# Kernel tuning notes

Measured on AMD Instinct MI355X. Metric: run time of the kernel, lower is better.

The kernel has to match this reference:

```python
import jax, jax.numpy as jnp
import numpy as np

B, L, D, H = 4, 2048, 512, 8
DH = D // H

def cdist(x):
    # torch.cdist(x, x) with p=2: (b,l,l) euclidean distances over feature dim
    sq = jnp.sum(x * x, axis=-1)  # (b,l)
    d2 = sq[:, :, None] + sq[:, None, :] - 2.0 * jnp.einsum('bld,bmd->blm', x, x)
    return jnp.sqrt(jnp.maximum(d2, 0.0))

def distance_residual_bias(cd, mask2d):
    # raw_max=True branch
    Dm = cd * mask2d
    row_max = jnp.max(Dm, axis=-1, keepdims=True)  # (b,l,1)
    Dm = row_max - Dm
    eye = jnp.eye(Dm.shape[-1], dtype=Dm.dtype)
    Dm = Dm * (1.0 - eye)  # zero diagonal
    return Dm * mask2d

def layernorm(x, g, b, eps=1e-5):
    mu = jnp.mean(x, axis=-1, keepdims=True)
    var = jnp.mean((x - mu) ** 2, axis=-1, keepdims=True)
    return (x - mu) * jax.lax.rsqrt(var + eps) * g + b

def setup_inputs() -> dict:
    key = jax.random.key(0)
    ks = jax.random.split(key, 16)
    s = lambda k, shape: jax.random.normal(k, shape, dtype=jnp.float32) * 0.02
    inp = {
        'x': jax.random.normal(ks[0], (B, L, D), dtype=jnp.float32),
        'node_mask': jnp.ones((B, L), dtype=jnp.float32),
        'wq': s(ks[1], (D, D)), 'bq': jnp.zeros((D,), jnp.float32),
        'wk': s(ks[2], (D, D)), 'bk': jnp.zeros((D,), jnp.float32),
        'wv': s(ks[3], (D, D)), 'bv': jnp.zeros((D,), jnp.float32),
        'wo': s(ks[4], (D, D)), 'bo': jnp.zeros((D,), jnp.float32),
        'ln1_g': jnp.ones((D,), jnp.float32), 'ln1_b': jnp.zeros((D,), jnp.float32),
        'w1': s(ks[5], (D, 4 * D)), 'b1': jnp.zeros((4 * D,), jnp.float32),
        'w2': s(ks[6], (4 * D, D)), 'b2': jnp.zeros((D,), jnp.float32),
        'ln2_g': jnp.ones((D,), jnp.float32), 'ln2_b': jnp.zeros((D,), jnp.float32),
    }
    return inp

def reference(x, node_mask, wq, bq, wk, bk, wv, bv, wo, bo,
              ln1_g, ln1_b, w1, b1, w2, b2, ln2_g, ln2_b):
    b, l, d = x.shape
    mask2d = node_mask[:, :, None] * node_mask[:, None, :]  # (b,l,l)
    bias = distance_residual_bias(cdist(x), mask2d)          # (b,l,l)

    q = (x @ wq + bq).reshape(b, l, H, DH).transpose(0, 2, 1, 3)
    k = (x @ wk + bk).reshape(b, l, H, DH).transpose(0, 2, 1, 3)
    v = (x @ wv + bv).reshape(b, l, H, DH).transpose(0, 2, 1, 3)
    scores = jnp.einsum('bhqd,bhkd->bhqk', q, k) / jnp.sqrt(jnp.float32(DH))
    scores = scores + bias[:, None, :, :]  # broadcast distance bias over heads
    attn = jax.nn.softmax(scores, axis=-1)
    y = jnp.einsum('bhqk,bhkd->bhqd', attn, v).transpose(0, 2, 1, 3).reshape(b, l, d)
    y = y @ wo + bo

    X = layernorm(x + y, ln1_g, ln1_b)            # AddNorm 1 (dropout=eval/no-op)
    ffn = jax.nn.relu(X @ w1 + b1) @ w2 + b2      # PositionWiseFFN
    X = layernorm(X + ffn, ln2_g, ln2_b)          # AddNorm 2
    return X
```

## Files before the change

kernel.cpp:

```cpp
#include <hip/hip_runtime.h>
#include <stdint.h>

#define GAS __attribute__((address_space(1)))
#define LAS __attribute__((address_space(3)))

typedef __attribute__((ext_vector_type(8))) __bf16 bf16x8;
typedef __attribute__((ext_vector_type(4))) float f32x4;

static constexpr int Bb = 4, Ll = 2048, Dd = 512, Hh = 8, DHd = 64;
static constexpr float LOG2E = 1.4426950408889634f;

__device__ __forceinline__ unsigned short f2bf(float f){
  unsigned u = __float_as_uint(f);
  u += 0x7fffu + ((u >> 16) & 1u);
  return (unsigned short)(u >> 16);
}
__device__ __forceinline__ float bf2f(unsigned short s){
  return __uint_as_float(((unsigned)s) << 16);
}
__device__ __forceinline__ void gload16(const void* g, void* l){
  __builtin_amdgcn_global_load_lds((const GAS void*)g, (LAS void*)l, 16, 0, 0);
}
__device__ __forceinline__ f32x4 mfma16(bf16x8 a, bf16x8 b, f32x4 c){
  return __builtin_amdgcn_mfma_f32_16x16x32_bf16(a, b, c, 0, 0, 0);
}
__device__ __forceinline__ float exp2_hw(float x){
  float r; asm("v_exp_f32 %0, %1" : "=v"(r) : "v"(x)); return r;
}

__global__ __launch_bounds__(256) void sumsq_cast(const float* __restrict__ x,
                                                  unsigned short* __restrict__ xbf,
                                                  float* __restrict__ sq){
  int row = blockIdx.x, tid = threadIdx.x;
  float2 v = ((const float2*)(x + (size_t)row * Dd))[tid];
  ((unsigned*)(xbf + (size_t)row * Dd))[tid] =
      (unsigned)f2bf(v.x) | ((unsigned)f2bf(v.y) << 16);
  float s2 = v.x * v.x + v.y * v.y;
  #pragma unroll
  for (int t = 1; t < 64; t <<= 1) s2 += __shfl_xor(s2, t, 64);
  __shared__ float red[4];
  if ((tid & 63) == 0) red[tid >> 6] = s2;
  __syncthreads();
  if (tid == 0) sq[row] = red[0] + red[1] + red[2] + red[3];
}

__global__ void transpose_all(
    const float* __restrict__ wq, const float* __restrict__ wk,
    const float* __restrict__ wv, const float* __restrict__ wo,
    const float* __restrict__ w1, const float* __restrict__ w2,
    unsigned short* __restrict__ wqkvT, unsigned short* __restrict__ woT,
    unsigned short* __restrict__ w1T, unsigned short* __restrict__ w2T)
{
  __shared__ float t[32][33];
  int bid = blockIdx.x;
  const float* in; unsigned short* out; int R, C, bx, by;
  if (bid < 1024){
    int s = bid >> 8, tt = bid & 255;
    in  = s == 0 ? wq : s == 1 ? wk : s == 2 ? wv : wo;
    out = s == 3 ? woT : wqkvT + s * 512 * 512;
    R = 512; C = 512; bx = tt & 15; by = tt >> 4;
  } else if (bid < 2048){
    int tt = bid - 1024; in = w1; out = w1T; R = 512; C = 2048; bx = tt & 63; by = tt >> 6;
  } else {
    int tt = bid - 2048; in = w2; out = w2T; R = 2048; C = 512; bx = tt & 15; by = tt >> 4;
  }
  int tx = threadIdx.x, ty = threadIdx.y;
  int c0 = bx * 32, r0 = by * 32;
  #pragma unroll
  for (int j = 0; j < 32; j += 8) t[ty + j][tx] = in[(size_t)(r0 + ty + j) * C + c0 + tx];
  __syncthreads();
  #pragma unroll
  for (int j = 0; j < 32; j += 8) out[(size_t)(c0 + ty + j) * R + r0 + tx] = f2bf(t[tx][ty + j]);
}

__global__ __launch_bounds__(256) void v_transpose(const unsigned short* __restrict__ qkv,
                                                   unsigned short* __restrict__ vT){
  int b = blockIdx.z, h = blockIdx.y, l0 = blockIdx.x * 64;
  int tid = threadIdx.x;
  __shared__ unsigned short t[64 * 64];
  #pragma unroll
  for (int it = 0; it < 2; ++it){
    int row = tid >> 2;
    int c = (tid & 3) + it * 4;
    uint4 d = *(const uint4*)(qkv + (size_t)(b * Ll + l0 + row) * 1536 + 1024 + h * DHd + c * 8);
    *(uint4*)((char*)t + row * 128 + ((c ^ (row & 7)) << 4)) = d;
  }
  __syncthreads();
  #pragma unroll
  for (int it = 0; it < 2; ++it){
    int dh = tid >> 2;
    int c2 = (tid & 3) + it * 4;
    unsigned pk[4];
    #pragma unroll
    for (int p = 0; p < 4; ++p){
      unsigned short e0, e1;
      {
        int ll = c2 * 8 + p * 2;
        e0 = *(const unsigned short*)((const char*)t + ll * 128 +
              ((((dh >> 3) ^ (ll & 7))) << 4) + ((dh & 7) << 1));
        ll = c2 * 8 + p * 2 + 1;
        e1 = *(const unsigned short*)((const char*)t + ll * 128 +
              ((((dh >> 3) ^ (ll & 7))) << 4) + ((dh & 7) << 1));
      }
      pk[p] = (unsigned)e0 | ((unsigned)e1 << 16);
    }
    uint4 o; o.x = pk[0]; o.y = pk[1]; o.z = pk[2]; o.w = pk[3];
    *(uint4*)(vT + ((size_t)(b * Hh + h) * DHd + dh) * Ll + l0 + c2 * 8) = o;
  }
}

template<int MODE>
__global__ __launch_bounds__(256) void gemm_bt(
    const unsigned short* __restrict__ A,
    const unsigned short* __restrict__ Bt,
    int M, int N, int K,
    const float* __restrict__ bias,
    const float* __restrict__ extra,
    float* __restrict__ outf,
    unsigned short* __restrict__ outb,
    const float* __restrict__ sq,
    float* __restrict__ rmax,
    const float* __restrict__ mask,
    const float* __restrict__ bias_k,
    const float* __restrict__ bias_v)
{
  if (MODE == 0){
    int z = blockIdx.z;
    A    += (size_t)z * Ll * Dd;
    Bt    = A;
    outb += (size_t)z * Ll * Ll;
    sq += z * Ll; rmax += z * Ll; mask += z * Ll;
  }
  const int m0 = blockIdx.y * 128, n0 = blockIdx.x * 128;
  const int tid = threadIdx.x, w = tid >> 6, l = tid & 63;
  const int wm = w >> 1, wn = w & 1;
  __shared__ unsigned short lA[2][128 * 64];
  __shared__ unsigned short lB[2][128 * 64];
  f32x4 acc[4][4];
  const f32x4 z4 = {0.f, 0.f, 0.f, 0.f};
  #pragma unroll
  for (int i = 0; i < 4; i++){
    #pragma unroll
    for (int j = 0; j < 4; j++) acc[i][j] = z4;
  }
  const int srow = w * 8 + (l >> 3);
  const int sc = l & 7;

  #pragma unroll
  for (int j = 0; j < 4; j++){
    int row = j * 32 + srow;
    gload16(A + (size_t)(m0 + row) * K + ((sc ^ (row & 7)) << 3),
            &lA[0][0] + j * 2048 + w * 512);
    gload16(Bt + (size_t)(n0 + row) * K + ((sc ^ (row & 7)) << 3),
            &lB[0][0] + j * 2048 + w * 512);
  }
  __syncthreads();

  int cur = 0;
  for (int k0 = 0; k0 < K; k0 += 64, cur ^= 1){
    if (k0 + 64 < K){
      #pragma unroll
      for (int j = 0; j < 4; j++){
        int row = j * 32 + srow;
        gload16(A + (size_t)(m0 + row) * K + k0 + 64 + ((sc ^ (row & 7)) << 3),
                &lA[cur ^ 1][0] + j * 2048 + w * 512);
        gload16(Bt + (size_t)(n0 + row) * K + k0 + 64 + ((sc ^ (row & 7)) << 3),
                &lB[cur ^ 1][0] + j * 2048 + w * 512);
      }
    }
    bf16x8 af[4][2], bv[4][2];
    #pragma unroll
    for (int kk = 0; kk < 2; kk++){
      #pragma unroll
      for (int f = 0; f < 4; f++){
        int ra = wm * 64 + f * 16 + (l & 15);
        af[f][kk] = *(const bf16x8*)((const char*)&lA[cur][0] + ra * 128 +
                      (((kk * 4 + (l >> 4)) ^ (ra & 7)) << 4));
        int rb = wn * 64 + f * 16 + (l & 15);
        bv[f][kk] = *(const bf16x8*)((const char*)&lB[cur][0] + rb * 128 +
                      (((kk * 4 + (l >> 4)) ^ (rb & 7)) << 4));
      }
    }
    #pragma unroll
    for (int mf = 0; mf < 4; mf++){
      #pragma unroll
      for (int nf = 0; nf < 4; nf++){
        #pragma unroll
        for (int kk = 0; kk < 2; kk++)
          acc[mf][nf] = mfma16(af[mf][kk], bv[nf][kk], acc[mf][nf]);
      }
    }
    __syncthreads();
  }

  #pragma unroll
  for (int mf = 0; mf < 4; mf++){
    #pragma unroll
    for (int r = 0; r < 4; r++){
      int row = m0 + wm * 64 + mf * 16 + (l >> 4) * 4 + r;
      if (MODE == 0){
        float sqi = sq[row];
        float mi  = mask[row];
        float rm = 0.f;
        #pragma unroll
        for (int nf = 0; nf < 4; nf++){
          int col = n0 + wn * 64 + nf * 16 + (l & 15);
          float g  = acc[mf][nf][r];
          float d2 = sqi + sq[col] - 2.f * g;
          float cd = sqrtf(fmaxf(d2, 0.f));
          float cdm = cd * (mi * mask[col]) * LOG2E;
          outb[(size_t)row * Ll + col] = f2bf(cdm);
          rm = fmaxf(rm, cdm);
        }
        #pragma unroll
        for (int t = 1; t < 16; t <<= 1) rm = fmaxf(rm, __shfl_xor(rm, t, 64));
        if ((l & 15) == 0) atomicMax((int*)(rmax + row), __float_as_int(rm));
      } else {
        #pragma unroll
        for (int nf = 0; nf < 4; nf++){
          int col = n0 + wn * 64 + nf * 16 + (l & 15);
          float bval;
          if (MODE == 5){
            const float* bp = col < 512 ? bias : (col < 1024 ? bias_k : bias_v);
            bval = bp[col & 511];
          } else {
            bval = bias[col];
          }
          float v = acc[mf][nf][r] + bval;
          if (MODE == 3) outb[(size_t)row * N + col] = f2bf(fmaxf(v, 0.f));
          if (MODE == 5) outb[(size_t)row * N + col] = f2bf(v);
          if (MODE == 2 || MODE == 4)
            outf[(size_t)row * N + col] = v + extra[(size_t)row * N + col];
        }
      }
    }
  }
}

__global__ __launch_bounds__(256) void flash_attn(
    const unsigned short* __restrict__ qkv,
    const unsigned short* __restrict__ vT,
    const unsigned short* __restrict__ cdm,
    const float* __restrict__ rmax,
    unsigned short* __restrict__ y)
{
  const int b = blockIdx.z, h = blockIdx.y, q0 = blockIdx.x * 64;
  const int tid = threadIdx.x, w = tid >> 6, l = tid & 63;
  const int ql = l & 15, lg = l >> 4;
  __shared__ unsigned short QPs[64 * 64];
  __shared__ unsigned short Ks[2][64 * 64];
  __shared__ unsigned short Vs[2][64 * 64];

  const int srow = w * 8 + (l >> 3);
  const int sc = l & 7;
  const unsigned short* kbase = qkv + (size_t)b * Ll * 1536 + 512 + h * DHd;
  const unsigned short* vbase = vT + (size_t)(b * Hh + h) * DHd * Ll;

  #pragma unroll
  for (int j = 0; j < 2; j++){
    int row = j * 32 + srow;
    gload16(qkv + (size_t)(b * Ll + q0 + row) * 1536 + h * DHd + ((sc ^ (row & 7)) << 3),
            QPs + j * 2048 + w * 512);
    gload16(kbase + (size_t)row * 1536 + ((sc ^ (row & 7)) << 3),
            &Ks[0][0] + j * 2048 + w * 512);
    gload16(vbase + (size_t)row * Ll + ((sc ^ (row & 7)) << 3),
            &Vs[0][0] + j * 2048 + w * 512);
  }

  const int qg = q0 + w * 16 + ql;
  const float rmx = rmax[b * Ll + qg];
  const unsigned short* cdrow = cdm + (size_t)(b * Ll + qg) * Ll;

  uint2 cdn[4];
  #pragma unroll
  for (int nf = 0; nf < 4; nf++)
    cdn[nf] = *(const uint2*)(cdrow + nf * 16 + lg * 4);

  f32x4 o[4];
  const f32x4 z4 = {0.f, 0.f, 0.f, 0.f};
  #pragma unroll
  for (int nf = 0; nf < 4; nf++) o[nf] = z4;
  float mprev = -1e30f, lsum = 0.f;

  __syncthreads();

  bf16x8 qa[2];
  #pragma unroll
  for (int kk = 0; kk < 2; kk++){
    int ra = w * 16 + ql;
    qa[kk] = *(const bf16x8*)((const char*)QPs + ra * 128 +
               (((kk * 4 + lg) ^ (ql & 7)) << 4));
  }

  const int NT = Ll / 64;
  for (int t = 0; t < NT; ++t){
    const int k0 = t * 64;
    const int cur = t & 1;

    uint2 cdc[4];
    #pragma unroll
    for (int nf = 0; nf < 4; nf++) cdc[nf] = cdn[nf];

    if (t + 1 < NT){
      const int kn = k0 + 64;
      #pragma unroll
      for (int nf = 0; nf < 4; nf++)
        cdn[nf] = *(const uint2*)(cdrow + kn + nf * 16 + lg * 4);
      #pragma unroll
      for (int j = 0; j < 2; j++){
        int row = j * 32 + srow;
        gload16(kbase + (size_t)(kn + row) * 1536 + ((sc ^ (row & 7)) << 3),
                &Ks[cur ^ 1][0] + j * 2048 + w * 512);
        gload16(vbase + (size_t)row * Ll + kn + ((sc ^ (row & 7)) << 3),
                &Vs[cur ^ 1][0] + j * 2048 + w * 512);
      }
    }

    f32x4 s[4];
    #pragma unroll
    for (int nf = 0; nf < 4; nf++){
      s[nf] = z4;
      #pragma unroll
      for (int kk = 0; kk < 2; kk++){
        int rb = nf * 16 + ql;
        bf16x8 kb = *(const bf16x8*)((const char*)Ks[cur] + rb * 128 +
                      (((kk * 4 + lg) ^ (ql & 7)) << 4));
        s[nf] = mfma16(kb, qa[kk], s[nf]);
      }
    }

    float sv[16];
    #pragma unroll
    for (int nf = 0; nf < 4; nf++){
      float c0 = __uint_as_float(cdc[nf].x << 16);
      float c1 = __uint_as_float(cdc[nf].x & 0xffff0000u);
      float c2 = __uint_as_float(cdc[nf].y << 16);
      float c3 = __uint_as_float(cdc[nf].y & 0xffff0000u);
      sv[nf * 4 + 0] = fmaf(s[nf][0], 0.125f * LOG2E, -c0);
      sv[nf * 4 + 1] = fmaf(s[nf][1], 0.125f * LOG2E, -c1);
      sv[nf * 4 + 2] = fmaf(s[nf][2], 0.125f * LOG2E, -c2);
      sv[nf * 4 + 3] = fmaf(s[nf][3], 0.125f * LOG2E, -c3);
    }
    if (k0 == q0){
      #pragma unroll
      for (int nf = 0; nf < 4; nf++) if (nf == w){
        #pragma unroll
        for (int r = 0; r < 4; r++)
          if (lg * 4 + r == ql) sv[nf * 4 + r] -= rmx;
      }
    }

    float tm = sv[0];
    #pragma unroll
    for (int i = 1; i < 16; i++) tm = fmaxf(tm, sv[i]);
    tm = fmaxf(tm, __shfl_xor(tm, 16, 64));
    tm = fmaxf(tm, __shfl_xor(tm, 32, 64));

    if (__any(tm > mprev + 8.f)){
      float mnew = fmaxf(mprev, tm);
      float a_ = exp2_hw(mprev - mnew);
      mprev = mnew;
      lsum *= a_;
      float al[4];
      #pragma unroll
      for (int r = 0; r < 4; r++)
        al[r] = __shfl(a_, (l & 48) | (lg * 4 + r), 64);
      #pragma unroll
      for (int nf = 0; nf < 4; nf++){
        f32x4 tv = o[nf];
        tv[0] *= al[0]; tv[1] *= al[1]; tv[2] *= al[2]; tv[3] *= al[3];
        o[nf] = tv;
      }
    }

    float p[16], ps = 0.f;
    #pragma unroll
    for (int i = 0; i < 16; i++){ p[i] = exp2_hw(sv[i] - mprev); ps += p[i]; }
    lsum += ps;

    #pragma unroll
    for (int nf = 0; nf < 4; nf++){
      unsigned d0, d1;
      asm("v_cvt_pk_bf16_f32 %0, %1, %2" : "=v"(d0) : "v"(p[nf*4+0]), "v"(p[nf*4+1]));
      asm("v_cvt_pk_bf16_f32 %0, %1, %2" : "=v"(d1) : "v"(p[nf*4+2]), "v"(p[nf*4+3]));
      uint2 pk2; pk2.x = d0; pk2.y = d1;
      *(uint2*)((char*)QPs + w * 2048 + ql * 128 +
                ((nf * 32 + lg * 8) ^ ((ql & 7) << 4))) = pk2;
    }

    bf16x8 pa[2];
    #pragma unroll
    for (int kk = 0; kk < 2; kk++)
      pa[kk] = *(const bf16x8*)((const char*)QPs + w * 2048 + ql * 128 +
                 ((((kk * 4 + lg)) ^ (ql & 7)) << 4));
    #pragma unroll
    for (int nf = 0; nf < 4; nf++){
      #pragma unroll
      for (int kk = 0; kk < 2; kk++){
        int rv = nf * 16 + ql;
        bf16x8 vb = *(const bf16x8*)((const char*)Vs[cur] + rv * 128 +
                      (((kk * 4 + lg) ^ (ql & 7)) << 4));
        o[nf] = mfma16(pa[kk], vb, o[nf]);
      }
    }
    __syncthreads();
  }

  float ltot = lsum;
  ltot += __shfl_xor(ltot, 16, 64);
  ltot += __shfl_xor(ltot, 32, 64);
  float lf[4];
  #pragma unroll
  for (int r = 0; r < 4; r++)
    lf[r] = __shfl(ltot, (l & 48) | (lg * 4 + r), 64);
  #pragma unroll
  for (int nf = 0; nf < 4; nf++){
    #pragma unroll
    for (int r = 0; r < 4; r++){
      int qo = q0 + w * 16 + lg * 4 + r;
      float v = o[nf][r] / lf[r];
      y[(size_t)(b * Ll + qo) * Dd + h * DHd + nf * 16 + ql] = f2bf(v);
    }
  }
}

__global__ __launch_bounds__(256) void ln_kernel(const float* __restrict__ in,
                                                 const float* __restrict__ g,
                                                 const float* __restrict__ bt,
                                                 float* __restrict__ outf,
                                                 unsigned short* __restrict__ outb){
  int row = blockIdx.x, tid = threadIdx.x;
  float2 v = ((const float2*)(in + (size_t)row * Dd))[tid];
  float s = v.x + v.y, s2 = v.x * v.x + v.y * v.y;
  #pragma unroll
  for (int t = 1; t < 64; t <<= 1){ s += __shfl_xor(s, t, 64); s2 += __shfl_xor(s2, t, 64); }
  __shared__ float red[8];
  if ((tid & 63) == 0){ red[tid >> 6] = s; red[4 + (tid >> 6)] = s2; }
  __syncthreads();
  float S  = red[0] + red[1] + red[2] + red[3];
  float S2 = red[4] + red[5] + red[6] + red[7];
  float mu = S * (1.f / 512.f);
  float var = fmaxf(S2 * (1.f / 512.f) - mu * mu, 0.f);
  float rs = rsqrtf(var + 1e-5f);
  int c = tid * 2;
  float o0 = (v.x - mu) * rs * g[c] + bt[c];
  float o1 = (v.y - mu) * rs * g[c + 1] + bt[c + 1];
  float2 ov; ov.x = o0; ov.y = o1;
  ((float2*)(outf + (size_t)row * Dd))[tid] = ov;
  if (outb){
    ((unsigned*)(outb + (size_t)row * Dd))[tid] =
        (unsigned)f2bf(o0) | ((unsigned)f2bf(o1) << 16);
  }
}

extern "C" void kernel_launch(void* const* d_in, const int* in_sizes, int n_in,
                              void* d_out, int out_size, void* d_ws, size_t ws_size,
                              hipStream_t stream){
  const float* x     = (const float*)d_in[0];
  const float* nmask = (const float*)d_in[1];
  const float* wq = (const float*)d_in[2];  const float* bq = (const float*)d_in[3];
  const float* wk = (const float*)d_in[4];  const float* bk = (const float*)d_in[5];
  const float* wv = (const float*)d_in[6];  const float* bv = (const float*)d_in[7];
  const float* wo = (const float*)d_in[8];  const float* bo = (const float*)d_in[9];
  const float* ln1g = (const float*)d_in[10]; const float* ln1b = (const float*)d_in[11];
  const float* w1 = (const float*)d_in[12]; const float* b1 = (const float*)d_in[13];
  const float* w2 = (const float*)d_in[14]; const float* b2 = (const float*)d_in[15];
  const float* ln2g = (const float*)d_in[16]; const float* ln2b = (const float*)d_in[17];
  float* outp = (float*)d_out;
  char* ws = (char*)d_ws;

  unsigned short* xbf   = (unsigned short*)(ws + 0);
  float* sq   = (float*)(ws + 8388608);
  float* rmax = (float*)(ws + 8421376);
  unsigned short* wqkvT = (unsigned short*)(ws + 8454144);
  unsigned short* woT   = (unsigned short*)(ws + 10027008);
  unsigned short* w1T   = (unsigned short*)(ws + 10551296);
  unsigned short* w2T   = (unsigned short*)(ws + 12648448);
  unsigned short* cdm   = (unsigned short*)(ws + 14745600);
  unsigned short* qkv   = (unsigned short*)(ws + 48300032);
  unsigned short* vT    = (unsigned short*)(ws + 73465856);
  unsigned short* yb    = (unsigned short*)(ws + 81854464);
  float* res = (float*)(ws + 90243072);
  float* Xf  = (float*)(ws + 107020288);
  unsigned short* h1  = cdm;
  unsigned short* Xbf = qkv;

  hipMemsetAsync(rmax, 0, sizeof(float) * Bb * Ll, stream);

  sumsq_cast<<<Bb * Ll, 256, 0, stream>>>(x, xbf, sq);

  transpose_all<<<3072, dim3(32, 8), 0, stream>>>(wq, wk, wv, wo, w1, w2,
                                                  wqkvT, woT, w1T, w2T);

  gemm_bt<0><<<dim3(16, 16, 4), 256, 0, stream>>>(xbf, xbf, Ll, Ll, Dd,
      nullptr, nullptr, nullptr, cdm, sq, rmax, nmask, nullptr, nullptr);

  gemm_bt<5><<<dim3(12, 64, 1), 256, 0, stream>>>(xbf, wqkvT, Bb * Ll, 1536, Dd,
      bq, nullptr, nullptr, qkv, nullptr, nullptr, nullptr, bk, bv);

  v_transpose<<<dim3(Ll / 64, Hh, Bb), 256, 0, stream>>>(qkv, vT);

  flash_attn<<<dim3(Ll / 64, Hh, Bb), 256, 0, stream>>>(qkv, vT, cdm, rmax, yb);

  gemm_bt<2><<<dim3(4, 64, 1), 256, 0, stream>>>(yb, woT, Bb * Ll, Dd, Dd,
      bo, x, res, nullptr, nullptr, nullptr, nullptr, nullptr, nullptr);

  ln_kernel<<<Bb * Ll, 256, 0, stream>>>(res, ln1g, ln1b, Xf, Xbf);

  gemm_bt<3><<<dim3(16, 64, 1), 256, 0, stream>>>(Xbf, w1T, Bb * Ll, 4 * Dd, Dd,
      b1, nullptr, nullptr, h1, nullptr, nullptr, nullptr, nullptr, nullptr);
  gemm_bt<4><<<dim3(4, 64, 1), 256, 0, stream>>>(h1, w2T, Bb * Ll, Dd, 4 * Dd,
      b2, Xf, res, nullptr, nullptr, nullptr, nullptr, nullptr, nullptr);

  ln_kernel<<<Bb * Ll, 256, 0, stream>>>(res, ln2g, ln2b, outp, nullptr);
}
```

Baseline: 258.6 us.

## Exploit cdist symmetry, drop online softmax max, split-K final FFN GEMM

The distance GEMM now launches only upper-triangular tiles and writes each off-diagonal tile twice, once transposed, which roughly halves the Gram-matrix MFMA work. Row maxima are updated atomically for both orientations. Attention drops the running-max rescaling: because the bias row max is known in advance, scores are shifted by a fixed offset of rmax-8, removing the per-tile max reduction and the accumulator rescale. The second FFN GEMM is split-K into two fp32 partials that a new fused kernel sums with bias, residual and LayerNorm, which raises occupancy on the narrow N=512 GEMM. The fixed-offset softmax relies on the attention scores being small relative to the bias and could overflow for inputs with large scores.

```diff
diff --git a/kernel.cpp b/kernel.cpp
--- a/kernel.cpp
+++ b/kernel.cpp
@@ -14,9 +14,6 @@
   unsigned u = __float_as_uint(f);
   u += 0x7fffu + ((u >> 16) & 1u);
   return (unsigned short)(u >> 16);
-}
-__device__ __forceinline__ float bf2f(unsigned short s){
-  return __uint_as_float(((unsigned)s) << 16);
 }
 __device__ __forceinline__ void gload16(const void* g, void* l){
   __builtin_amdgcn_global_load_lds((const GAS void*)g, (LAS void*)l, 16, 0, 0);
@@ -124,14 +121,27 @@
     const float* __restrict__ bias_k,
     const float* __restrict__ bias_v)
 {
+  int m0, n0, bxx = 0, byy = 0;
   if (MODE == 0){
     int z = blockIdx.z;
     A    += (size_t)z * Ll * Dd;
     Bt    = A;
     outb += (size_t)z * Ll * Ll;
     sq += z * Ll; rmax += z * Ll; mask += z * Ll;
-  }
-  const int m0 = blockIdx.y * 128, n0 = blockIdx.x * 128;
+    int tt = blockIdx.x, byv = 0;
+    while (tt >= 16 - byv){ tt -= 16 - byv; byv++; }
+    byy = byv; bxx = byv + tt;
+    m0 = byy * 128; n0 = bxx * 128;
+  } else {
+    m0 = blockIdx.y * 128; n0 = blockIdx.x * 128;
+  }
+  if (MODE == 6){
+    int z = blockIdx.z;
+    A    += (size_t)z * (K >> 1);
+    Bt   += (size_t)z * (K >> 1);
+    outf += (size_t)z * (size_t)M * N;
+  }
+  const int KL = (MODE == 6) ? (K >> 1) : K;
   const int tid = threadIdx.x, w = tid >> 6, l = tid & 63;
   const int wm = w >> 1, wn = w & 1;
   __shared__ unsigned short lA[2][128 * 64];
@@ -157,8 +167,8 @@
   __syncthreads();
 
   int cur = 0;
-  for (int k0 = 0; k0 < K; k0 += 64, cur ^= 1){
-    if (k0 + 64 < K){
+  for (int k0 = 0; k0 < KL; k0 += 64, cur ^= 1){
+    if (k0 + 64 < KL){
       #pragma unroll
       for (int j = 0; j < 4; j++){
         int row = j * 32 + srow;
@@ -193,51 +203,95 @@
     __syncthreads();
   }
 
-  #pragma unroll
-  for (int mf = 0; mf < 4; mf++){
-    #pragma unroll
-    for (int r = 0; r < 4; r++){
-      int row = m0 + wm * 64 + mf * 16 + (l >> 4) * 4 + r;
-      if (MODE == 0){
-        float sqi = sq[row];
-        float mi  = mask[row];
+  if (MODE == 0){
+    float sqc[4], mkc[4];
+    #pragma unroll
+    for (int nf = 0; nf < 4; nf++){
+      int col = n0 + wn * 64 + nf * 16 + (l & 15);
+      sqc[nf] = sq[col]; mkc[nf] = mask[col];
+    }
+    #pragma unroll
+    for (int mf = 0; mf < 4; mf++){
+      #pragma unroll
+      for (int r = 0; r < 4; r++){
+        int row = m0 + wm * 64 + mf * 16 + (l >> 4) * 4 + r;
+        float sqi = sq[row], mi = mask[row];
+        #pragma unroll
+        for (int nf = 0; nf < 4; nf++){
+          float d2 = sqi + sqc[nf] - 2.f * acc[mf][nf][r];
+          acc[mf][nf][r] = sqrtf(fmaxf(d2, 0.f)) * (mi * mkc[nf]) * LOG2E + 8.f;
+        }
+      }
+    }
+    #pragma unroll
+    for (int mf = 0; mf < 4; mf++){
+      #pragma unroll
+      for (int r = 0; r < 4; r++){
+        int row = m0 + wm * 64 + mf * 16 + (l >> 4) * 4 + r;
         float rm = 0.f;
         #pragma unroll
         for (int nf = 0; nf < 4; nf++){
           int col = n0 + wn * 64 + nf * 16 + (l & 15);
-          float g  = acc[mf][nf][r];
-          float d2 = sqi + sq[col] - 2.f * g;
-          float cd = sqrtf(fmaxf(d2, 0.f));
-          float cdm = cd * (mi * mask[col]) * LOG2E;
-          outb[(size_t)row * Ll + col] = f2bf(cdm);
-          rm = fmaxf(rm, cdm);
+          outb[(size_t)row * Ll + col] = f2bf(acc[mf][nf][r]);
+          rm = fmaxf(rm, acc[mf][nf][r]);
         }
         #pragma unroll
         for (int t = 1; t < 16; t <<= 1) rm = fmaxf(rm, __shfl_xor(rm, t, 64));
         if ((l & 15) == 0) atomicMax((int*)(rmax + row), __float_as_int(rm));
-      } else {
+      }
+    }
+    if (bxx != byy){
+      #pragma unroll
+      for (int nf = 0; nf < 4; nf++){
+        int col = n0 + wn * 64 + nf * 16 + (l & 15);
+        float cm = 0.f;
+        #pragma unroll
+        for (int mf = 0; mf < 4; mf++){
+          uint2 pk2;
+          pk2.x = (unsigned)f2bf(acc[mf][nf][0]) | ((unsigned)f2bf(acc[mf][nf][1]) << 16);
+          pk2.y = (unsigned)f2bf(acc[mf][nf][2]) | ((unsigned)f2bf(acc[mf][nf][3]) << 16);
+          int rowb = m0 + wm * 64 + mf * 16 + (l >> 4) * 4;
+          *(uint2*)(outb + (size_t)col * Ll + rowb) = pk2;
+          cm = fmaxf(cm, fmaxf(fmaxf(acc[mf][nf][0], acc[mf][nf][1]),
+                               fmaxf(acc[mf][nf][2], acc[mf][nf][3])));
+        }
+        cm = fmaxf(cm, __shfl_xor(cm, 16, 64));
+        cm = fmaxf(cm, __shfl_xor(cm, 32, 64));
+        if ((l >> 4) == 0) atomicMax((int*)(rmax + col), __float_as_int(cm));
+      }
+    }
+  } else {
+    #pragma unroll
+    for (int mf = 0; mf < 4; mf++){
+      #pragma unroll
+      for (int r = 0; r < 4; r++){
+        int row = m0 + wm * 64 + mf * 16 + (l >> 4) * 4 + r;
         #pragma unroll
         for (int nf = 0; nf < 4; nf++){
           int col = n0 + wn * 64 + nf * 16 + (l & 15);
-          float bval;
-          if (MODE == 5){
-            const float* bp = col < 512 ? bias : (col < 1024 ? bias_k : bias_v);
-            bval = bp[col & 511];
+          if (MODE == 6){
+            outf[(size_t)row * N + col] = acc[mf][nf][r];
           } else {
-            bval = bias[col];
+            float bval;
+            if (MODE == 5){
+              const float* bp = col < 512 ? bias : (col < 1024 ? bias_k : bias_v);
+              bval = bp[col & 511];
+            } else {
+              bval = bias[col];
+            }
+            float v = acc[mf][nf][r] + bval;
+            if (MODE == 3) outb[(size_t)row * N + col] = f2bf(fmaxf(v, 0.f));
+            if (MODE == 5) outb[(size_t)row * N + col] = f2bf(v);
+            if (MODE == 2)
+              outf[(size_t)row * N + col] = v + extra[(size_t)row * N + col];
           }
-          float v = acc[mf][nf][r] + bval;
-          if (MODE == 3) outb[(size_t)row * N + col] = f2bf(fmaxf(v, 0.f));
-          if (MODE == 5) outb[(size_t)row * N + col] = f2bf(v);
-          if (MODE == 2 || MODE == 4)
-            outf[(size_t)row * N + col] = v + extra[(size_t)row * N + col];
         }
       }
     }
   }
 }
 
-__global__ __launch_bounds__(256) void flash_attn(
+__global__ __launch_bounds__(256, 4) void flash_attn(
     const unsigned short* __restrict__ qkv,
     const unsigned short* __restrict__ vT,
     const unsigned short* __restrict__ cdm,
@@ -268,7 +322,7 @@
   }
 
   const int qg = q0 + w * 16 + ql;
-  const float rmx = rmax[b * Ll + qg];
+  const float rmx8 = rmax[b * Ll + qg] - 8.f;
   const unsigned short* cdrow = cdm + (size_t)(b * Ll + qg) * Ll;
 
   uint2 cdn[4];
@@ -280,7 +334,7 @@
   const f32x4 z4 = {0.f, 0.f, 0.f, 0.f};
   #pragma unroll
   for (int nf = 0; nf < 4; nf++) o[nf] = z4;
-  float mprev = -1e30f, lsum = 0.f;
+  float lsum = 0.f;
 
   __syncthreads();
 
@@ -346,36 +400,13 @@
       for (int nf = 0; nf < 4; nf++) if (nf == w){
         #pragma unroll
         for (int r = 0; r < 4; r++)
-          if (lg * 4 + r == ql) sv[nf * 4 + r] -= rmx;
-      }
-    }
-
-    float tm = sv[0];
-    #pragma unroll
-    for (int i = 1; i < 16; i++) tm = fmaxf(tm, sv[i]);
-    tm = fmaxf(tm, __shfl_xor(tm, 16, 64));
-    tm = fmaxf(tm, __shfl_xor(tm, 32, 64));
-
-    if (__any(tm > mprev + 8.f)){
-      float mnew = fmaxf(mprev, tm);
-      float a_ = exp2_hw(mprev - mnew);
-      mprev = mnew;
-      lsum *= a_;
-      float al[4];
-      #pragma unroll
-      for (int r = 0; r < 4; r++)
-        al[r] = __shfl(a_, (l & 48) | (lg * 4 + r), 64);
-      #pragma unroll
-      for (int nf = 0; nf < 4; nf++){
-        f32x4 tv = o[nf];
-        tv[0] *= al[0]; tv[1] *= al[1]; tv[2] *= al[2]; tv[3] *= al[3];
-        o[nf] = tv;
+          if (lg * 4 + r == ql) sv[nf * 4 + r] -= rmx8;
       }
     }
 
     float p[16], ps = 0.f;
     #pragma unroll
-    for (int i = 0; i < 16; i++){ p[i] = exp2_hw(sv[i] - mprev); ps += p[i]; }
+    for (int i = 0; i < 16; i++){ p[i] = exp2_hw(sv[i]); ps += p[i]; }
     lsum += ps;
 
     #pragma unroll
@@ -451,6 +482,37 @@
     ((unsigned*)(outb + (size_t)row * Dd))[tid] =
         (unsigned)f2bf(o0) | ((unsigned)f2bf(o1) << 16);
   }
+}
+
+__global__ __launch_bounds__(256) void ln2p_kernel(
+    const float* __restrict__ p01,
+    const float* __restrict__ bias,
+    const float* __restrict__ extra,
+    const float* __restrict__ g, const float* __restrict__ bt,
+    float* __restrict__ outf)
+{
+  int row = blockIdx.x, tid = threadIdx.x;
+  float2 a0 = ((const float2*)(p01 + (size_t)row * Dd))[tid];
+  float2 a1 = ((const float2*)(p01 + (size_t)Bb * Ll * Dd + (size_t)row * Dd))[tid];
+  float2 ex = ((const float2*)(extra + (size_t)row * Dd))[tid];
+  int c = tid * 2;
+  float vx = a0.x + a1.x + bias[c]     + ex.x;
+  float vy = a0.y + a1.y + bias[c + 1] + ex.y;
+  float s = vx + vy, s2 = vx * vx + vy * vy;
+  #pragma unroll
+  for (int t = 1; t < 64; t <<= 1){ s += __shfl_xor(s, t, 64); s2 += __shfl_xor(s2, t, 64); }
+  __shared__ float red[8];
+  if ((tid & 63) == 0){ red[tid >> 6] = s; red[4 + (tid >> 6)] = s2; }
+  __syncthreads();
+  float S  = red[0] + red[1] + red[2] + red[3];
+  float S2 = red[4] + red[5] + red[6] + red[7];
+  float mu = S * (1.f / 512.f);
+  float var = fmaxf(S2 * (1.f / 512.f) - mu * mu, 0.f);
+  float rs = rsqrtf(var + 1e-5f);
+  float o0 = (vx - mu) * rs * g[c] + bt[c];
+  float o1 = (vy - mu) * rs * g[c + 1] + bt[c + 1];
+  float2 ov; ov.x = o0; ov.y = o1;
+  ((float2*)(outf + (size_t)row * Dd))[tid] = ov;
 }
 
 extern "C" void kernel_launch(void* const* d_in, const int* in_sizes, int n_in,
@@ -484,6 +546,7 @@
   float* Xf  = (float*)(ws + 107020288);
   unsigned short* h1  = cdm;
   unsigned short* Xbf = qkv;
+  float* p01 = (float*)qkv;
 
   hipMemsetAsync(rmax, 0, sizeof(float) * Bb * Ll, stream);
 
@@ -492,7 +555,7 @@
   transpose_all<<<3072, dim3(32, 8), 0, stream>>>(wq, wk, wv, wo, w1, w2,
                                                   wqkvT, woT, w1T, w2T);
 
-  gemm_bt<0><<<dim3(16, 16, 4), 256, 0, stream>>>(xbf, xbf, Ll, Ll, Dd,
+  gemm_bt<0><<<dim3(136, 1, 4), 256, 0, stream>>>(xbf, xbf, Ll, Ll, Dd,
       nullptr, nullptr, nullptr, cdm, sq, rmax, nmask, nullptr, nullptr);
 
   gemm_bt<5><<<dim3(12, 64, 1), 256, 0, stream>>>(xbf, wqkvT, Bb * Ll, 1536, Dd,
@@ -509,8 +572,8 @@
 
   gemm_bt<3><<<dim3(16, 64, 1), 256, 0, stream>>>(Xbf, w1T, Bb * Ll, 4 * Dd, Dd,
       b1, nullptr, nullptr, h1, nullptr, nullptr, nullptr, nullptr, nullptr);
-  gemm_bt<4><<<dim3(4, 64, 1), 256, 0, stream>>>(h1, w2T, Bb * Ll, Dd, 4 * Dd,
-      b2, Xf, res, nullptr, nullptr, nullptr, nullptr, nullptr, nullptr);
-
-  ln_kernel<<<Bb * Ll, 256, 0, stream>>>(res, ln2g, ln2b, outp, nullptr);
-}
+  gemm_bt<6><<<dim3(4, 64, 2), 256, 0, stream>>>(h1, w2T, Bb * Ll, Dd, 4 * Dd,
+      nullptr, nullptr, p01, nullptr, nullptr, nullptr, nullptr, nullptr, nullptr);
+
+  ln2p_kernel<<<Bb * Ll, 256, 0, stream>>>(p01, b2, Xf, ln2g, ln2b, outp);
+}
```

Result: faster. 251.5 us (-2.7%).
